# Performance work log

Hardware: AMD Instinct MI355X
Metric: run time of the kernel (lower is better)

The kernel has to match this reference:

```python
import jax, jax.numpy as jnp
import numpy as np

B, T, E, H, V = 64, 32, 300, 1024, 10000


def setup_inputs() -> dict:
    key = jax.random.key(0)
    ks = jax.random.split(key, 12)
    s = lambda fan: 1.0 / np.sqrt(fan)
    return {
        "questions": jax.random.randint(ks[0], (B, T), 0, V, dtype=jnp.int64) if jax.config.jax_enable_x64 else jax.random.randint(ks[0], (B, T), 0, V, dtype=jnp.int32),
        "question_lengths": jax.random.randint(ks[1], (B,), 1, T + 1, dtype=jnp.int32),
        "embed_table": jax.random.normal(ks[2], (V, E), jnp.float32) * 0.02,
        "W_ih1": jax.random.normal(ks[3], (4 * H, E), jnp.float32) * s(H),
        "W_hh1": jax.random.normal(ks[4], (4 * H, H), jnp.float32) * s(H),
        "b_ih1": jax.random.normal(ks[5], (4 * H,), jnp.float32) * s(H),
        "b_hh1": jax.random.normal(ks[6], (4 * H,), jnp.float32) * s(H),
        "W_ih2": jax.random.normal(ks[7], (4 * H, H), jnp.float32) * s(H),
        "W_hh2": jax.random.normal(ks[8], (4 * H, H), jnp.float32) * s(H),
        "b_ih2": jax.random.normal(ks[9], (4 * H,), jnp.float32) * s(H),
        "b_hh2": jax.random.normal(ks[10], (4 * H,), jnp.float32) * s(H),
    }


def _lstm_cell(x_t, h, c, W_ih, W_hh, b_ih, b_hh):
    # PyTorch LSTMCell: gate order i, f, g, o
    gates = x_t @ W_ih.T + b_ih + h @ W_hh.T + b_hh  # [B, 4H]
    i, f, g, o = jnp.split(gates, 4, axis=-1)
    c_new = jax.nn.sigmoid(f) * c + jax.nn.sigmoid(i) * jnp.tanh(g)
    h_new = jax.nn.sigmoid(o) * jnp.tanh(c_new)
    return h_new, c_new


def reference(questions, question_lengths, embed_table,
              W_ih1, W_hh1, b_ih1, b_hh1, W_ih2, W_hh2, b_ih2, b_hh2):
    x = embed_table[questions]                      # [B, T, E]
    b, t, _ = x.shape
    h = W_hh1.shape[1]

    def step(carry, inp):
        h1, c1, h2, c2 = carry
        x_t, m = inp                                # x_t [B,E], m [B,1] bool
        h1n, c1n = _lstm_cell(x_t, h1, c1, W_ih1, W_hh1, b_ih1, b_hh1)
        h2n, c2n = _lstm_cell(h1n, h2, c2, W_ih2, W_hh2, b_ih2, b_hh2)
        # samples past their length keep their final state frozen
        h1 = jnp.where(m, h1n, h1); c1 = jnp.where(m, c1n, c1)
        h2 = jnp.where(m, h2n, h2); c2 = jnp.where(m, c2n, c2)
        return (h1, c1, h2, c2), None

    mask = jnp.arange(t)[None, :] < question_lengths[:, None]      # [B,T]
    xs = (jnp.swapaxes(x, 0, 1), jnp.swapaxes(mask, 0, 1)[..., None])
    init = tuple(jnp.zeros((b, h), x.dtype) for _ in range(4))
    (h1, c1, h2, c2), _ = jax.lax.scan(step, init, xs)

    # tile final top-layer hidden to [B, H, 28, 28]
    E_q = jnp.broadcast_to(h2[:, None, None, :], (b, 28, 28, h))
    E_q = jnp.transpose(E_q, (0, 3, 2, 1))
    return (E_q, h1[:, None, :], h2[:, None, :], c1[:, None, :], c2[:, None, :])
```

## Files before the change

kernel.cpp:

```cpp
#include <hip/hip_runtime.h>
#include <hip/hip_bf16.h>
#include <cstdint>

#define B_  64
#define T_  32
#define E_  300
#define EP  320
#define H_  1024
#define G4  4096
#define BH  65536
#define NBLK 256

#define EQOFF 0LL
#define H1OFF 51380224LL
#define H2OFF 51445760LL
#define C1OFF 51511296LL
#define C2OFF 51576832LL

typedef __attribute__((ext_vector_type(8))) short bf16x8;
typedef __attribute__((ext_vector_type(4))) float f32x4;
typedef unsigned short ushort_t;

__device__ __forceinline__ bf16x8 load_b8(const ushort_t* p) {
    union { uint4 u; bf16x8 v; } c;
    c.u = *reinterpret_cast<const uint4*>(p);
    return c.v;
}

__device__ __forceinline__ ushort_t f2bf(float x) {
    union { float f; uint32_t u; } c; c.f = x;
    uint32_t r = c.u + 0x7fffu + ((c.u >> 16) & 1u);
    return (ushort_t)(r >> 16);
}

__device__ __forceinline__ float sigm(float x) { return 1.0f / (1.0f + __expf(-x)); }

__device__ __forceinline__ void astore64(uint64_t* p, uint64_t v) {
    __hip_atomic_store(p, v, __ATOMIC_RELAXED, __HIP_MEMORY_SCOPE_AGENT);
}
__device__ __forceinline__ void astoref(float* p, float v) {
    __hip_atomic_store(p, v, __ATOMIC_RELAXED, __HIP_MEMORY_SCOPE_AGENT);
}
__device__ __forceinline__ uint64_t packf2(float a, float b) {
    union { float f[2]; uint64_t u; } c; c.f[0] = a; c.f[1] = b; return c.u;
}

__device__ __forceinline__ void setflag(int* flags, int role, int js, int val) {
    __hip_atomic_store(&flags[(role * 64 + js) * 16], val,
                       __ATOMIC_RELAXED, __HIP_MEMORY_SCOPE_AGENT);
}
__device__ __forceinline__ void waitwave(const int* flags, int role, int target, int lane) {
    const int* p = &flags[(role * 64 + lane) * 16];
    int guard = 0;
    for (;;) {
        int v = __hip_atomic_load(p, __ATOMIC_RELAXED, __HIP_MEMORY_SCOPE_AGENT);
        if (__all(v >= target)) return;
        if (++guard > (1 << 22)) return;
        __builtin_amdgcn_s_sleep(1);
    }
}

__global__ void prep_inputs(const int* __restrict__ q, const float* __restrict__ table,
                            ushort_t* __restrict__ Xp,
                            const float* __restrict__ Wsrc, ushort_t* __restrict__ Wdst,
                            ushort_t* __restrict__ h1s0, ushort_t* __restrict__ h2s0,
                            int* __restrict__ flags) {
    int blk = blockIdx.x;
    if (blk < 1280) {
        int i = blk * 256 + threadIdx.x;
        const int n = B_ * T_ * EP;
        for (; i < n; i += 1280 * 256) {
            int r = i / EP, c = i - r * EP;
            Xp[i] = (c < E_) ? f2bf(table[q[r] * E_ + c]) : (ushort_t)0;
        }
    } else if (blk < 3328) {
        int i = (blk - 1280) * 256 + threadIdx.x;
        const int n = G4 * EP;
        for (; i < n; i += 2048 * 256) {
            int r = i / EP, c = i - r * EP;
            Wdst[i] = (c < E_) ? f2bf(Wsrc[r * E_ + c]) : (ushort_t)0;
        }
    } else if (blk < 3392) {
        int i = (blk - 3328) * 256 + threadIdx.x;
        uint4 z = make_uint4(0, 0, 0, 0);
        if (i < 8192) reinterpret_cast<uint4*>(h1s0)[i] = z;
        else          reinterpret_cast<uint4*>(h2s0)[i - 8192] = z;
    } else {
        int i = (blk - 3392) * 256 + threadIdx.x;
        reinterpret_cast<uint4*>(flags)[i] = make_uint4(0, 0, 0, 0);
    }
}

__launch_bounds__(256)
__global__ void xgemm(const ushort_t* __restrict__ Xp, const ushort_t* __restrict__ Wp,
                      const float* __restrict__ b_ih1, const float* __restrict__ b_hh1,
                      float* __restrict__ xg) {
    int mblk = blockIdx.x, nblk = blockIdx.y;
    int wave = threadIdx.x >> 6, lane = threadIdx.x & 63;
    int lm = lane & 15, lq = lane >> 4;
    int m0 = mblk * 64 + wave * 16;
    f32x4 acc[4];
    #pragma unroll
    for (int g = 0; g < 4; ++g) {
        int n = nblk * 64 + g * 16 + lm;
        float bv = b_ih1[n] + b_hh1[n];
        acc[g] = (f32x4){bv, bv, bv, bv};
    }
    for (int k0 = 0; k0 < EP; k0 += 32) {
        bf16x8 a = load_b8(Xp + (m0 + lm) * EP + k0 + lq * 8);
        #pragma unroll
        for (int g = 0; g < 4; ++g) {
            bf16x8 b = load_b8(Wp + (nblk * 64 + g * 16 + lm) * EP + k0 + lq * 8);
            acc[g] = __builtin_amdgcn_mfma_f32_16x16x32_bf16(a, b, acc[g], 0, 0, 0);
        }
    }
    #pragma unroll
    for (int g = 0; g < 4; ++g)
        #pragma unroll
        for (int r = 0; r < 4; ++r) {
            int m = m0 + lq * 4 + r;
            int b = m >> 5, t = m & 31;
            int n = nblk * 64 + g * 16 + lm;
            int gate = n >> 10, j = n & 1023;
            xg[(((size_t)t * B_ + b) * H_ + j) * 4 + gate] = acc[g][r];
        }
}


__device__ __forceinline__ void gemm_half(const ushort_t* __restrict__ hslot,
                                          const ushort_t* __restrict__ wsf,
                                          int lm, int lq, int m0, int kh, f32x4 acc[4]) {
    const uint4* hr = reinterpret_cast<const uint4*>(hslot);
    const int rbase = (m0 + lm) * 2 + (lq & 1);
    const int cbo = lq >> 1;
    const int cb0 = kh * 32;
    uint4 buf[16];
    #pragma unroll
    for (int grp = 0; grp < 2; ++grp)
        #pragma unroll
        for (int i = 0; i < 8; ++i)
            buf[grp * 8 + i] = hr[(cb0 + grp * 16 + i * 2 + cbo) * 128 + rbase];
    #pragma unroll
    for (int grp = 0; grp < 2; ++grp)
        #pragma unroll
        for (int i = 0; i < 8; ++i) {
            int k0 = kh * 512 + grp * 256 + i * 32;
            union { uint4 u; bf16x8 v; } a; a.u = buf[grp * 8 + i];
            #pragma unroll
            for (int g = 0; g < 4; ++g) {
                int row = g * 16 + lm;
                bf16x8 bb = load_b8(wsf + row * 1024 + ((k0 + lq * 8) ^ ((lm & 7) << 3)));
                acc[g] = __builtin_amdgcn_mfma_f32_16x16x32_bf16(a.v, bb, acc[g], 0, 0, 0);
            }
        }
}

__device__ __forceinline__ void lstm_elem(const f32x4 acc[4], int r,
                                          float* c, float* h, ushort_t* hb) {
    float iv = sigm(acc[0][r]);
    float fv = sigm(acc[1][r]);
    float gv = tanhf(acc[2][r]);
    float ov = sigm(acc[3][r]);
    float cn = fv * c[r] + iv * gv;
    float hv = ov * tanhf(cn);
    c[r] = cn; h[r] = hv; hb[r] = f2bf(hv);
}

__device__ __forceinline__ void store_h_tile(ushort_t* slot, int js, const ushort_t* hst) {
    int tid = threadIdx.x;
    uint64_t v = reinterpret_cast<const uint64_t*>(hst)[tid];
    astore64(reinterpret_cast<uint64_t*>(slot) + js * 256 + tid, v);
}

__global__ __launch_bounds__(512) void lstm_persist(
    const float* __restrict__ Whh1, const float* __restrict__ Wih2,
    const float* __restrict__ Whh2,
    const float* __restrict__ b_ih2, const float* __restrict__ b_hh2,
    const float* __restrict__ xg, const int* __restrict__ qlen,
    ushort_t* __restrict__ h1hist,
    ushort_t* __restrict__ h2hist,
    float* __restrict__ Qhist,
    float* __restrict__ h2f,
    float* __restrict__ out,
    int* __restrict__ flags)
{
    __shared__ ushort_t ws[64 * 1024];
    __shared__ __align__(16) ushort_t hstage[64][16];
    __shared__ f32x4 pacc[256][4];
    __shared__ int qlen_sh[64];

    const int blk  = blockIdx.x;
    const int role = blk >> 6;
    const int js   = blk & 63;
    const int w    = threadIdx.x >> 6, lane = threadIdx.x & 63;
    const int mi   = w & 3, kh = w >> 2;
    const int lm = lane & 15, lq = lane >> 4;
    const int m0 = mi * 16;
    const int pidx = mi * 64 + lane;

    if (threadIdx.x < 64) qlen_sh[threadIdx.x] = qlen[threadIdx.x];

    if (role == 3) {
        __syncthreads();
        for (int t = 0; t < T_; ++t) {
            bool any = false;
            for (int b = 0; b < B_; ++b) any |= (qlen_sh[b] == t + 1);
            if (!any) continue;
            if (threadIdx.x == 0) {
                const int* p = &flags[(2 * 64 + js) * 16];
                int guard = 0;
                while (__hip_atomic_load(p, __ATOMIC_RELAXED, __HIP_MEMORY_SCOPE_AGENT) < t + 1) {
                    if (++guard > (1 << 22)) break;
                    __builtin_amdgcn_s_sleep(1);
                }
            }
            __syncthreads();
            for (int b = 0; b < B_; ++b) {
                if (qlen_sh[b] != t + 1) continue;
                const float* src = h2f + (size_t)b * H_ + js * 16;
                f32x4* dst = reinterpret_cast<f32x4*>(
                    out + (size_t)b * (H_ * 784) + (size_t)js * 16 * 784);
                for (int idx = threadIdx.x; idx < 3136; idx += 512) {
                    int c = idx / 196, p4 = idx - c * 196;
                    float v = src[c];
                    f32x4 vv = (f32x4){v, v, v, v};
                    __builtin_nontemporal_store(vv, &dst[c * 196 + p4]);
                }
            }
        }
        return;
    }

    const float* Wsrc = (role == 0) ? Whh1 : (role == 1) ? Wih2 : Whh2;
    uint2* wsp = reinterpret_cast<uint2*>(ws);
    for (int idx = threadIdx.x; idx < 64 * 256; idx += 512) {
        int r = idx >> 8, c4 = idx & 255;
        int grow = (r >> 4) * H_ + js * 16 + (r & 15);
        float4 v = reinterpret_cast<const float4*>(Wsrc + (size_t)grow * H_)[c4];
        uint2 pk;
        pk.x = (uint32_t)f2bf(v.x) | ((uint32_t)f2bf(v.y) << 16);
        pk.y = (uint32_t)f2bf(v.z) | ((uint32_t)f2bf(v.w) << 16);
        wsp[r * 256 + (c4 ^ ((r & 7) << 1))] = pk;
    }
    __syncthreads();

    int q[4];
    #pragma unroll
    for (int r = 0; r < 4; ++r) q[r] = qlen_sh[m0 + lq * 4 + r];

    float    c_reg[4]  = {0.f, 0.f, 0.f, 0.f};
    float    h_reg[4]  = {0.f, 0.f, 0.f, 0.f};
    ushort_t hb_reg[4] = {0, 0, 0, 0};

    if (role == 0) {
        for (int t = 0; t < T_; ++t) {
            f32x4 acc[4];
            #pragma unroll
            for (int g = 0; g < 4; ++g) acc[g] = (f32x4){0.f, 0.f, 0.f, 0.f};
            if (kh == 0) {
                uint4 xq[4];
                #pragma unroll
                for (int r = 0; r < 4; ++r)
                    xq[r] = reinterpret_cast<const uint4*>(xg)
                            [((size_t)t * B_ + (m0 + lq * 4 + r)) * H_ + js * 16 + lm];
                #pragma unroll
                for (int r = 0; r < 4; ++r) {
                    union { uint32_t u; float f; } x0, x1, x2, x3;
                    x0.u = xq[r].x; x1.u = xq[r].y; x2.u = xq[r].z; x3.u = xq[r].w;
                    acc[0][r] = x0.f; acc[1][r] = x1.f;
                    acc[2][r] = x2.f; acc[3][r] = x3.f;
                }
            }
            if (t > 0) {
                if (w == 0) waitwave(flags, 0, t, lane);
                __syncthreads();
            }
            gemm_half(h1hist + (size_t)t * BH, ws, lm, lq, m0, kh, acc);
            if (kh == 1) {
                #pragma unroll
                for (int g = 0; g < 4; ++g) pacc[pidx][g] = acc[g];
            }
            __syncthreads();
            if (kh == 0) {
                #pragma unroll
                for (int g = 0; g < 4; ++g) acc[g] += pacc[pidx][g];
                #pragma unroll
                for (int r = 0; r < 4; ++r) {
                    if (t < q[r]) lstm_elem(acc, r, c_reg, h_reg, hb_reg);
                    hstage[m0 + lq * 4 + r][lm] = hb_reg[r];
                    if (q[r] == t + 1) {
                        int b = m0 + lq * 4 + r, j = js * 16 + lm;
                        __builtin_nontemporal_store(h_reg[r], &out[H1OFF + b * H_ + j]);
                        __builtin_nontemporal_store(c_reg[r], &out[C1OFF + b * H_ + j]);
                    }
                }
            }
            __syncthreads();
            if (threadIdx.x < 256)
                store_h_tile(h1hist + (size_t)(t + 1) * BH, js, &hstage[0][0]);
            __syncthreads();
            if (threadIdx.x == 0) setflag(flags, 0, js, t + 1);
        }
    } else if (role == 1) {
        float bi[4];
        #pragma unroll
        for (int g = 0; g < 4; ++g) {
            int n = g * H_ + js * 16 + lm;
            bi[g] = b_ih2[n] + b_hh2[n];
        }
        for (int t = 0; t < T_; ++t) {
            if (w == 0) waitwave(flags, 0, t + 1, lane);
            __syncthreads();
            f32x4 acc[4];
            #pragma unroll
            for (int g = 0; g < 4; ++g)
                acc[g] = (kh == 0) ? (f32x4){bi[g], bi[g], bi[g], bi[g]}
                                   : (f32x4){0.f, 0.f, 0.f, 0.f};
            gemm_half(h1hist + (size_t)(t + 1) * BH, ws, lm, lq, m0, kh, acc);
            if (kh == 1) {
                #pragma unroll
                for (int g = 0; g < 4; ++g) pacc[pidx][g] = acc[g];
            }
            __syncthreads();
            if (kh == 0) {
                #pragma unroll
                for (int g = 0; g < 4; ++g) acc[g] += pacc[pidx][g];
                uint64_t* Qw64 = (uint64_t*)(Qhist + (size_t)t * (4 * BH));
                #pragma unroll
                for (int r = 0; r < 4; ++r) {
                    int b = m0 + lq * 4 + r, j = js * 16 + lm;
                    size_t base = ((size_t)b * H_ + j) * 2;
                    astore64(Qw64 + base,     packf2(acc[0][r], acc[1][r]));
                    astore64(Qw64 + base + 1, packf2(acc[2][r], acc[3][r]));
                }
            }
            __syncthreads();
            if (threadIdx.x == 0) setflag(flags, 1, js, t + 1);
        }
    } else {
        for (int t = 0; t < T_; ++t) {
            if (w == 0)               waitwave(flags, 1, t + 1, lane);
            else if (w == 1 && t > 0) waitwave(flags, 2, t,     lane);
            __syncthreads();
            uint4 qp[4];
            if (kh == 0) {
                const uint4* Qr = (const uint4*)(Qhist + (size_t)t * (4 * BH));
                #pragma unroll
                for (int r = 0; r < 4; ++r)
                    qp[r] = Qr[(size_t)(m0 + lq * 4 + r) * H_ + js * 16 + lm];
            }
            f32x4 acc[4];
            #pragma unroll
            for (int g = 0; g < 4; ++g) acc[g] = (f32x4){0.f, 0.f, 0.f, 0.f};
            gemm_half(h2hist + (size_t)t * BH, ws, lm, lq, m0, kh, acc);
            if (kh == 1) {
                #pragma unroll
                for (int g = 0; g < 4; ++g) pacc[pidx][g] = acc[g];
            }
            __syncthreads();
            if (kh == 0) {
                #pragma unroll
                for (int g = 0; g < 4; ++g) acc[g] += pacc[pidx][g];
                #pragma unroll
                for (int r = 0; r < 4; ++r) {
                    union { uint32_t u; float f; } x0, x1, x2, x3;
                    x0.u = qp[r].x; x1.u = qp[r].y; x2.u = qp[r].z; x3.u = qp[r].w;
                    acc[0][r] += x0.f; acc[1][r] += x1.f;
                    acc[2][r] += x2.f; acc[3][r] += x3.f;
                }
                #pragma unroll
                for (int r = 0; r < 4; ++r) {
                    if (t < q[r]) lstm_elem(acc, r, c_reg, h_reg, hb_reg);
                    hstage[m0 + lq * 4 + r][lm] = hb_reg[r];
                    if (q[r] == t + 1) {
                        int b = m0 + lq * 4 + r, j = js * 16 + lm;
                        astoref(&h2f[(size_t)b * H_ + j], h_reg[r]);
                        __builtin_nontemporal_store(h_reg[r], &out[H2OFF + b * H_ + j]);
                        __builtin_nontemporal_store(c_reg[r], &out[C2OFF + b * H_ + j]);
                    }
                }
            }
            __syncthreads();
            if (threadIdx.x < 256)
                store_h_tile(h2hist + (size_t)(t + 1) * BH, js, &hstage[0][0]);
            __syncthreads();
            if (threadIdx.x == 0) setflag(flags, 2, js, t + 1);
        }
    }
}

extern "C" void kernel_launch(void* const* d_in, const int* in_sizes, int n_in,
                              void* d_out, int out_size, void* d_ws, size_t ws_size,
                              hipStream_t stream) {
    const int*   questions = (const int*)d_in[0];
    const int*   qlen      = (const int*)d_in[1];
    const float* embed     = (const float*)d_in[2];
    const float* W_ih1     = (const float*)d_in[3];
    const float* W_hh1     = (const float*)d_in[4];
    const float* b_ih1     = (const float*)d_in[5];
    const float* b_hh1     = (const float*)d_in[6];
    const float* W_ih2     = (const float*)d_in[7];
    const float* W_hh2     = (const float*)d_in[8];
    const float* b_ih2     = (const float*)d_in[9];
    const float* b_hh2     = (const float*)d_in[10];
    float* out = (float*)d_out;

    char* w = (char*)d_ws;
    float*    xg     = (float*)(w + 0);
    ushort_t* Wih1p  = (ushort_t*)(w + 33554432);
    ushort_t* Xp     = (ushort_t*)(w + 36175872);
    ushort_t* h1hist = (ushort_t*)(w + 37486592);
    ushort_t* h2hist = (ushort_t*)(w + 41811968);
    float*    Qhist  = (float*)(w + 46137344);
    float*    h2f    = (float*)(w + 80216064);
    int*      flags  = (int*)(w + 80740352);

    prep_inputs<<<3395, 256, 0, stream>>>(questions, embed, Xp, W_ih1, Wih1p,
                                          h1hist, h2hist, flags);
    xgemm<<<dim3(32, 64), 256, 0, stream>>>(Xp, Wih1p, b_ih1, b_hh1, xg);

    lstm_persist<<<NBLK, 512, 0, stream>>>(W_hh1, W_ih2, W_hh2, b_ih2, b_hh2,
                                           xg, qlen,
                                           h1hist, h2hist, Qhist,
                                           h2f, out, flags);
}
```

Before: 541.4 us.

## Replace dedicated E_q broadcast blocks with a post-recurrence broadcast across all blocks

Removes the fourth role of 64 blocks that wrote the tiled E_q output incrementally as each sample finished, shrinking the grid from 256 to 192 blocks. After the recurrence, every block waits until all layer-2 flags reach the final step, then writes its contiguous slice of the 51 MB broadcast output from h2f. This drops the idle polling blocks and spreads the large store over all blocks, but the whole broadcast now runs after the recurrence instead of overlapping with it.

```diff
diff --git a/kernel.cpp b/kernel.cpp
--- a/kernel.cpp
+++ b/kernel.cpp
@@ -9,13 +9,15 @@
 #define H_  1024
 #define G4  4096
 #define BH  65536
-#define NBLK 256
+#define NBLK 192
 
 #define EQOFF 0LL
 #define H1OFF 51380224LL
 #define H2OFF 51445760LL
 #define C1OFF 51511296LL
 #define C2OFF 51576832LL
+#define EQ4TOT 12845056
+#define EQ4PB  66902
 
 typedef __attribute__((ext_vector_type(8))) short bf16x8;
 typedef __attribute__((ext_vector_type(4))) float f32x4;
@@ -200,37 +202,6 @@
 
     if (threadIdx.x < 64) qlen_sh[threadIdx.x] = qlen[threadIdx.x];
 
-    if (role == 3) {
-        __syncthreads();
-        for (int t = 0; t < T_; ++t) {
-            bool any = false;
-            for (int b = 0; b < B_; ++b) any |= (qlen_sh[b] == t + 1);
-            if (!any) continue;
-            if (threadIdx.x == 0) {
-                const int* p = &flags[(2 * 64 + js) * 16];
-                int guard = 0;
-                while (__hip_atomic_load(p, __ATOMIC_RELAXED, __HIP_MEMORY_SCOPE_AGENT) < t + 1) {
-                    if (++guard > (1 << 22)) break;
-                    __builtin_amdgcn_s_sleep(1);
-                }
-            }
-            __syncthreads();
-            for (int b = 0; b < B_; ++b) {
-                if (qlen_sh[b] != t + 1) continue;
-                const float* src = h2f + (size_t)b * H_ + js * 16;
-                f32x4* dst = reinterpret_cast<f32x4*>(
-                    out + (size_t)b * (H_ * 784) + (size_t)js * 16 * 784);
-                for (int idx = threadIdx.x; idx < 3136; idx += 512) {
-                    int c = idx / 196, p4 = idx - c * 196;
-                    float v = src[c];
-                    f32x4 vv = (f32x4){v, v, v, v};
-                    __builtin_nontemporal_store(vv, &dst[c * 196 + p4]);
-                }
-            }
-        }
-        return;
-    }
-
     const float* Wsrc = (role == 0) ? Whh1 : (role == 1) ? Wih2 : Whh2;
     uint2* wsp = reinterpret_cast<uint2*>(ws);
     for (int idx = threadIdx.x; idx < 64 * 256; idx += 512) {
@@ -385,6 +356,20 @@
                 store_h_tile(h2hist + (size_t)(t + 1) * BH, js, &hstage[0][0]);
             __syncthreads();
             if (threadIdx.x == 0) setflag(flags, 2, js, t + 1);
+        }
+    }
+
+    if (w == 0) waitwave(flags, 2, 32, lane);
+    __syncthreads();
+    {
+        const int start4 = blk * EQ4PB;
+        const int end4   = (start4 + EQ4PB < EQ4TOT) ? start4 + EQ4PB : EQ4TOT;
+        f32x4* eq = reinterpret_cast<f32x4*>(out);
+        for (int i4 = start4 + threadIdx.x; i4 < end4; i4 += 512) {
+            int bj = i4 / 196;
+            float v = h2f[bj];
+            f32x4 vv = (f32x4){v, v, v, v};
+            __builtin_nontemporal_store(vv, &eq[i4]);
         }
     }
 }
```

Measured after the change: 543.8 us. About the same (+0.4%).
